# Optimization experiments

Hardware: AMD Instinct MI355X
Metric: run time of the kernel (lower is better)

## Reference

```python
import jax, jax.numpy as jnp
import numpy as np

N_HEADS = 4
D_K = 64
SCALE = D_K ** (-0.5)


def setup_inputs() -> dict:
    key = jax.random.key(0)
    k1, k2, k3, k4, k5 = jax.random.split(key, 5)
    B, C, H, W = 16, 256, 32, 32
    x = jax.random.normal(k1, (B, C, H, W), dtype=jnp.float32)
    # Linear weights stored as (in, out) for x @ W convention
    w_qkv = jax.random.normal(k2, (C, N_HEADS * D_K * 3), dtype=jnp.float32) * (C ** -0.5)
    b_qkv = jax.random.normal(k3, (N_HEADS * D_K * 3,), dtype=jnp.float32) * 0.02
    w_out = jax.random.normal(k4, (N_HEADS * D_K, C), dtype=jnp.float32) * ((N_HEADS * D_K) ** -0.5)
    b_out = jax.random.normal(k5, (C,), dtype=jnp.float32) * 0.02
    return {"x": x, "w_qkv": w_qkv, "b_qkv": b_qkv, "w_out": w_out, "b_out": b_out}


def reference(x, w_qkv, b_qkv, w_out, b_out):
    # NOTE: the original torch module defines GroupNorm but never applies it
    # in forward; we faithfully reproduce the forward as written.
    B, C, H, W = x.shape
    S = H * W
    xs = x.reshape(B, C, S).transpose(0, 2, 1)            # [B, S, C]
    qkv = (xs @ w_qkv + b_qkv).reshape(B, S, N_HEADS, 3 * D_K)
    q, k, v = jnp.split(qkv, 3, axis=-1)                   # each [B, S, H, d_k]
    attn = jnp.einsum('bihd,bjhd->bijh', q, k) * SCALE     # [B, S, S, H]
    attn = jax.nn.softmax(attn, axis=2)                    # softmax over j (keys)
    res = jnp.einsum('bijh,bjhd->bihd', attn, v)           # [B, S, H, d_k]
    res = res.reshape(B, S, N_HEADS * D_K)
    res = res @ w_out + b_out + xs                         # residual add
    return res.transpose(0, 2, 1).reshape(B, C, H, W)
```

## Files before the change

### kernel.cpp

```cpp
#include <hip/hip_runtime.h>
#include <hip/hip_bf16.h>

typedef __attribute__((ext_vector_type(8))) short short8;
typedef __attribute__((ext_vector_type(4))) short short4v;
typedef __attribute__((ext_vector_type(4))) float floatx4;
typedef unsigned short u16;

#define SCL_LOG2E 0.1803368801111204f

__device__ inline u16 f2b(float f) {
  __hip_bfloat16 h = __float2bfloat16(f);
  union { __hip_bfloat16 h; u16 u; } cv; cv.h = h; return cv.u;
}

__global__ __launch_bounds__(256) void qkv_gemm(const float* __restrict__ x,
                                                const float* __restrict__ wq,
                                                const float* __restrict__ bias,
                                                u16* __restrict__ Qo,
                                                u16* __restrict__ Ko,
                                                u16* __restrict__ Vto) {
  __shared__ u16 As[128 * 40];
  __shared__ u16 Bs[128 * 40];
  const int tid = threadIdx.x, wave = tid >> 6, lane = tid & 63;
  const int l15 = lane & 15, quad = lane >> 4;
  const int wm = (wave >> 1) * 64, wn = (wave & 1) * 64;
  const int n0 = blockIdx.x * 128, m0 = blockIdx.y * 128;
  const int bb = m0 >> 10, s0 = m0 & 1023;
  const int c4 = (tid & 7) * 4;
  const int r4 = (tid >> 3) * 4;

  floatx4 acc[4][4] = {};

  for (int kt = 0; kt < 256; kt += 32) {
    const float* xr = x + ((size_t)(bb * 256 + kt + c4)) * 1024 + s0 + r4;
    const float* wr = wq + (size_t)(kt + c4) * 768 + n0 + r4;
    float4 av[4], bv[4];
#pragma unroll
    for (int i = 0; i < 4; i++) {
      av[i] = *(const float4*)&xr[(size_t)i * 1024];
      bv[i] = *(const float4*)&wr[(size_t)i * 768];
    }
#pragma unroll
    for (int j = 0; j < 4; j++) {
      ushort4 pa, pb;
      pa.x = f2b(((const float*)&av[0])[j]);
      pa.y = f2b(((const float*)&av[1])[j]);
      pa.z = f2b(((const float*)&av[2])[j]);
      pa.w = f2b(((const float*)&av[3])[j]);
      pb.x = f2b(((const float*)&bv[0])[j]);
      pb.y = f2b(((const float*)&bv[1])[j]);
      pb.z = f2b(((const float*)&bv[2])[j]);
      pb.w = f2b(((const float*)&bv[3])[j]);
      *(ushort4*)&As[(r4 + j) * 40 + c4] = pa;
      *(ushort4*)&Bs[(r4 + j) * 40 + c4] = pb;
    }
    __syncthreads();
    short8 af[4], bfr[4];
#pragma unroll
    for (int mi = 0; mi < 4; mi++)
      af[mi] = *(short8*)&As[(wm + mi * 16 + l15) * 40 + quad * 8];
#pragma unroll
    for (int ni = 0; ni < 4; ni++)
      bfr[ni] = *(short8*)&Bs[(wn + ni * 16 + l15) * 40 + quad * 8];
#pragma unroll
    for (int mi = 0; mi < 4; mi++)
#pragma unroll
      for (int ni = 0; ni < 4; ni++)
        acc[mi][ni] = __builtin_amdgcn_mfma_f32_16x16x32_bf16(af[mi], bfr[ni],
                                                              acc[mi][ni], 0, 0, 0);
    __syncthreads();
  }

#pragma unroll
  for (int ni = 0; ni < 4; ni++) {
    int n = n0 + wn + ni * 16 + l15;
    float bvv = bias[n];
    int h = n / 192;
    int rem = n - h * 192;
#pragma unroll
    for (int mi = 0; mi < 4; mi++) {
      int gm = m0 + wm + mi * 16 + quad * 4;
      int s = gm & 1023;
      if (rem < 128) {
        u16* dst;
        float scl;
        if (rem < 64) { dst = Qo; scl = SCL_LOG2E; } else { dst = Ko; scl = 1.0f; }
        int d = rem & 63;
#pragma unroll
        for (int r = 0; r < 4; r++)
          dst[((size_t)(bb * 4 + h) * 1024 + s + r) * 64 + d] =
              f2b((acc[mi][ni][r] + bvv) * scl);
      } else {
        int d = rem - 128;
        ushort4 pk;
        pk.x = f2b(acc[mi][ni][0] + bvv);
        pk.y = f2b(acc[mi][ni][1] + bvv);
        pk.z = f2b(acc[mi][ni][2] + bvv);
        pk.w = f2b(acc[mi][ni][3] + bvv);
        *(ushort4*)&Vto[((size_t)(bb * 4 + h) * 64 + d) * 1024 + s] = pk;
      }
    }
  }
}

__global__ __launch_bounds__(256, 2) void attn_kern(const u16* __restrict__ Q,
                                                    const u16* __restrict__ K,
                                                    const u16* __restrict__ Vt,
                                                    u16* __restrict__ O) {
  __shared__ u16 kv[2 * 2 * 64 * 72];
  const int bh = blockIdx.y;
  const u16* Qp = Q + (size_t)bh * 64 * 1024;
  const u16* Kp = K + (size_t)bh * 64 * 1024;
  const u16* Vp = Vt + (size_t)bh * 64 * 1024;
  u16* Op = O + (size_t)bh * 64 * 1024;
  const int q0 = blockIdx.x * 128;
  const int tid = threadIdx.x, wave = tid >> 6, lane = tid & 63;
  const int l15 = lane & 15, quad = lane >> 4;

  short8 qa[2][2];
#pragma unroll
  for (int qi = 0; qi < 2; qi++)
#pragma unroll
    for (int kh = 0; kh < 2; kh++)
      qa[qi][kh] = *(const short8*)&Qp[(size_t)(q0 + wave * 32 + qi * 16 + l15) * 64 +
                                       kh * 32 + quad * 8];

  const int srow = tid >> 2;
  const int sc = (tid & 3) * 16;

  {
    short8 k0 = *(const short8*)&Kp[(size_t)srow * 64 + sc];
    short8 k1 = *(const short8*)&Kp[(size_t)srow * 64 + sc + 8];
    short8 v0 = *(const short8*)&Vp[(size_t)srow * 1024 + sc];
    short8 v1 = *(const short8*)&Vp[(size_t)srow * 1024 + sc + 8];
    *(short8*)&kv[srow * 72 + sc] = k0;
    *(short8*)&kv[srow * 72 + sc + 8] = k1;
    *(short8*)&kv[4608 + srow * 72 + sc] = v0;
    *(short8*)&kv[4608 + srow * 72 + sc + 8] = v1;
  }
  __syncthreads();

  float lsum[2] = {0.f, 0.f};
  floatx4 acc[2][4] = {};

  for (int t = 0; t < 16; t++) {
    const u16* Ksb = kv + (t & 1) * 9216;
    const u16* Vsb = Ksb + 4608;

    short8 nk0, nk1, nv0, nv1;
    if (t < 15) {
      nk0 = *(const short8*)&Kp[(size_t)((t + 1) * 64 + srow) * 64 + sc];
      nk1 = *(const short8*)&Kp[(size_t)((t + 1) * 64 + srow) * 64 + sc + 8];
      nv0 = *(const short8*)&Vp[(size_t)srow * 1024 + (t + 1) * 64 + sc];
      nv1 = *(const short8*)&Vp[(size_t)srow * 1024 + (t + 1) * 64 + sc + 8];
    }

    short8 kb[4][2];
#pragma unroll
    for (int mj = 0; mj < 4; mj++)
#pragma unroll
      for (int kh = 0; kh < 2; kh++)
        kb[mj][kh] = *(const short8*)&Ksb[(mj * 16 + l15) * 72 + kh * 32 + quad * 8];

    floatx4 sf[2][4];
#pragma unroll
    for (int qi = 0; qi < 2; qi++)
#pragma unroll
      for (int mj = 0; mj < 4; mj++) {
        floatx4 z = {};
        z = __builtin_amdgcn_mfma_f32_16x16x32_bf16(kb[mj][0], qa[qi][0], z, 0, 0, 0);
        sf[qi][mj] =
            __builtin_amdgcn_mfma_f32_16x16x32_bf16(kb[mj][1], qa[qi][1], z, 0, 0, 0);
      }

    short4v pb[2][4];
#pragma unroll
    for (int qi = 0; qi < 2; qi++)
#pragma unroll
      for (int mj = 0; mj < 4; mj++) {
        float p0 = exp2f(sf[qi][mj][0]), p1 = exp2f(sf[qi][mj][1]);
        float p2 = exp2f(sf[qi][mj][2]), p3 = exp2f(sf[qi][mj][3]);
        lsum[qi] += (p0 + p1) + (p2 + p3);
        short4v pk;
        pk[0] = (short)f2b(p0); pk[1] = (short)f2b(p1);
        pk[2] = (short)f2b(p2); pk[3] = (short)f2b(p3);
        pb[qi][mj] = pk;
      }

#pragma unroll
    for (int c = 0; c < 4; c++)
#pragma unroll
      for (int md = 0; md < 4; md++) {
        short4v va = *(const short4v*)&Vsb[(md * 16 + l15) * 72 + c * 16 + quad * 4];
#pragma unroll
        for (int qi = 0; qi < 2; qi++)
          acc[qi][md] =
              __builtin_amdgcn_mfma_f32_16x16x16bf16_1k(va, pb[qi][c], acc[qi][md],
                                                        0, 0, 0);
      }

    if (t < 15) {
      u16* dst = kv + ((t + 1) & 1) * 9216;
      *(short8*)&dst[srow * 72 + sc] = nk0;
      *(short8*)&dst[srow * 72 + sc + 8] = nk1;
      *(short8*)&dst[4608 + srow * 72 + sc] = nv0;
      *(short8*)&dst[4608 + srow * 72 + sc + 8] = nv1;
    }
    __syncthreads();
  }

  float inv[2];
#pragma unroll
  for (int qi = 0; qi < 2; qi++) {
    lsum[qi] += __shfl_xor(lsum[qi], 16, 64);
    lsum[qi] += __shfl_xor(lsum[qi], 32, 64);
    inv[qi] = 1.f / lsum[qi];
  }

  __syncthreads();
  u16* Ot = kv;
#pragma unroll
  for (int qi = 0; qi < 2; qi++)
#pragma unroll
    for (int md = 0; md < 4; md++) {
      uint2 pk;
      u16 a0 = f2b(acc[qi][md][0] * inv[qi]), a1 = f2b(acc[qi][md][1] * inv[qi]);
      u16 a2 = f2b(acc[qi][md][2] * inv[qi]), a3 = f2b(acc[qi][md][3] * inv[qi]);
      pk.x = (unsigned)a0 | ((unsigned)a1 << 16);
      pk.y = (unsigned)a2 | ((unsigned)a3 << 16);
      *(uint2*)&Ot[(wave * 32 + qi * 16 + l15) * 72 + md * 16 + quad * 4] = pk;
    }
  __syncthreads();
#pragma unroll
  for (int rr = 0; rr < 4; rr++) {
    int row = wave * 32 + (lane >> 3) + 8 * rr;
    int col = (lane & 7) * 8;
    short8 v = *(const short8*)&Ot[row * 72 + col];
    *(short8*)&Op[(size_t)(q0 + row) * 64 + col] = v;
  }
}

__global__ __launch_bounds__(256) void out_gemm(const u16* __restrict__ Oin,
                                                const float* __restrict__ wo,
                                                const float* __restrict__ bias,
                                                const float* __restrict__ x,
                                                float* __restrict__ out) {
  __shared__ u16 As[64 * 32];
  __shared__ u16 Bs[128 * 40];
  const int tid = threadIdx.x, wave = tid >> 6, lane = tid & 63;
  const int l15 = lane & 15, quad = lane >> 4;
  const int wm = (wave >> 1) * 32, wn = (wave & 1) * 64;
  const int n0 = blockIdx.x * 128, m0 = blockIdx.y * 64;
  const int bb = m0 >> 10, s0 = m0 & 1023;
  const int ar = tid >> 2, ach = (tid & 3) * 8;
  const int c4 = (tid & 7) * 4, r4 = (tid >> 3) * 4;

  floatx4 acc[2][4] = {};

  for (int kt = 0; kt < 256; kt += 32) {
    int h = kt >> 6, d0 = kt & 63;
    *(short8*)&As[ar * 32 + ach] =
        *(const short8*)&Oin[((size_t)(bb * 4 + h) * 1024 + s0 + ar) * 64 + d0 + ach];
    const float* wr = wo + (size_t)(kt + c4) * 256 + n0 + r4;
    float4 bv[4];
#pragma unroll
    for (int i = 0; i < 4; i++) bv[i] = *(const float4*)&wr[(size_t)i * 256];
#pragma unroll
    for (int j = 0; j < 4; j++) {
      ushort4 pb;
      pb.x = f2b(((const float*)&bv[0])[j]);
      pb.y = f2b(((const float*)&bv[1])[j]);
      pb.z = f2b(((const float*)&bv[2])[j]);
      pb.w = f2b(((const float*)&bv[3])[j]);
      *(ushort4*)&Bs[(r4 + j) * 40 + c4] = pb;
    }
    __syncthreads();
    short8 af[2], bfr[4];
#pragma unroll
    for (int mi = 0; mi < 2; mi++)
      af[mi] = *(short8*)&As[(wm + mi * 16 + l15) * 32 + quad * 8];
#pragma unroll
    for (int ni = 0; ni < 4; ni++)
      bfr[ni] = *(short8*)&Bs[(wn + ni * 16 + l15) * 40 + quad * 8];
#pragma unroll
    for (int mi = 0; mi < 2; mi++)
#pragma unroll
      for (int ni = 0; ni < 4; ni++)
        acc[mi][ni] = __builtin_amdgcn_mfma_f32_16x16x32_bf16(af[mi], bfr[ni],
                                                              acc[mi][ni], 0, 0, 0);
    __syncthreads();
  }

#pragma unroll
  for (int ni = 0; ni < 4; ni++) {
    int c = n0 + wn + ni * 16 + l15;
    float bvv = bias[c];
#pragma unroll
    for (int mi = 0; mi < 2; mi++) {
      int gm = m0 + wm + mi * 16 + quad * 4;
      int s = gm & 1023;
      size_t idx = ((size_t)bb * 256 + c) * 1024 + s;
      float4 xr = *(const float4*)&x[idx];
      float4 o;
      o.x = acc[mi][ni][0] + bvv + xr.x;
      o.y = acc[mi][ni][1] + bvv + xr.y;
      o.z = acc[mi][ni][2] + bvv + xr.z;
      o.w = acc[mi][ni][3] + bvv + xr.w;
      *(float4*)&out[idx] = o;
    }
  }
}

extern "C" void kernel_launch(void* const* d_in, const int* in_sizes, int n_in,
                              void* d_out, int out_size, void* d_ws, size_t ws_size,
                              hipStream_t stream) {
  const float* x     = (const float*)d_in[0];
  const float* w_qkv = (const float*)d_in[1];
  const float* b_qkv = (const float*)d_in[2];
  const float* w_out = (const float*)d_in[3];
  const float* b_out = (const float*)d_in[4];
  float* out = (float*)d_out;
  char* ws = (char*)d_ws;

  u16* Qb  = (u16*)(ws);
  u16* Kb  = (u16*)(ws + 8388608);
  u16* Vtb = (u16*)(ws + 16777216);
  u16* Ob  = (u16*)(ws + 25165824);

  qkv_gemm<<<dim3(6, 128), 256, 0, stream>>>(x, w_qkv, b_qkv, Qb, Kb, Vtb);
  attn_kern<<<dim3(8, 64), 256, 0, stream>>>(Qb, Kb, Vtb, Ob);
  out_gemm<<<dim3(2, 256), 256, 0, stream>>>(Ob, w_out, b_out, x, out);
}
```

Baseline: 151.0 us.

## Halve attention query tile per block and swap GEMM grid axes

The attention kernel now processes 64 queries per block (16 per wave) instead of 128, doubling the grid to 1024 blocks and raising the occupancy hint to 4 blocks per CU. This aims to fill more CUs and hide latency, but each K/V tile loaded into shared memory is reused by half as many queries, so K/V traffic roughly doubles. Both GEMMs swap grid axes so consecutive blocks walk along M while sharing the same weight column tile, which should change L2 reuse patterns.

```diff
diff --git a/kernel.cpp b/kernel.cpp
--- a/kernel.cpp
+++ b/kernel.cpp
@@ -24,7 +24,7 @@
   const int tid = threadIdx.x, wave = tid >> 6, lane = tid & 63;
   const int l15 = lane & 15, quad = lane >> 4;
   const int wm = (wave >> 1) * 64, wn = (wave & 1) * 64;
-  const int n0 = blockIdx.x * 128, m0 = blockIdx.y * 128;
+  const int m0 = blockIdx.x * 128, n0 = blockIdx.y * 128;
   const int bb = m0 >> 10, s0 = m0 & 1023;
   const int c4 = (tid & 7) * 4;
   const int r4 = (tid >> 3) * 4;
@@ -103,7 +103,7 @@
   }
 }
 
-__global__ __launch_bounds__(256, 2) void attn_kern(const u16* __restrict__ Q,
+__global__ __launch_bounds__(256, 4) void attn_kern(const u16* __restrict__ Q,
                                                     const u16* __restrict__ K,
                                                     const u16* __restrict__ Vt,
                                                     u16* __restrict__ O) {
@@ -113,17 +113,14 @@
   const u16* Kp = K + (size_t)bh * 64 * 1024;
   const u16* Vp = Vt + (size_t)bh * 64 * 1024;
   u16* Op = O + (size_t)bh * 64 * 1024;
-  const int q0 = blockIdx.x * 128;
+  const int q0 = blockIdx.x * 64;
   const int tid = threadIdx.x, wave = tid >> 6, lane = tid & 63;
   const int l15 = lane & 15, quad = lane >> 4;
 
-  short8 qa[2][2];
-#pragma unroll
-  for (int qi = 0; qi < 2; qi++)
-#pragma unroll
-    for (int kh = 0; kh < 2; kh++)
-      qa[qi][kh] = *(const short8*)&Qp[(size_t)(q0 + wave * 32 + qi * 16 + l15) * 64 +
-                                       kh * 32 + quad * 8];
+  short8 qa[2];
+#pragma unroll
+  for (int kh = 0; kh < 2; kh++)
+    qa[kh] = *(const short8*)&Qp[(size_t)(q0 + wave * 16 + l15) * 64 + kh * 32 + quad * 8];
 
   const int srow = tid >> 2;
   const int sc = (tid & 3) * 16;
@@ -140,8 +137,8 @@
   }
   __syncthreads();
 
-  float lsum[2] = {0.f, 0.f};
-  floatx4 acc[2][4] = {};
+  float lsum = 0.f;
+  floatx4 acc[4] = {};
 
   for (int t = 0; t < 16; t++) {
     const u16* Ksb = kv + (t & 1) * 9216;
@@ -155,48 +152,34 @@
       nv1 = *(const short8*)&Vp[(size_t)srow * 1024 + (t + 1) * 64 + sc + 8];
     }
 
-    short8 kb[4][2];
-#pragma unroll
-    for (int mj = 0; mj < 4; mj++)
-#pragma unroll
-      for (int kh = 0; kh < 2; kh++)
-        kb[mj][kh] = *(const short8*)&Ksb[(mj * 16 + l15) * 72 + kh * 32 + quad * 8];
-
-    floatx4 sf[2][4];
-#pragma unroll
-    for (int qi = 0; qi < 2; qi++)
-#pragma unroll
-      for (int mj = 0; mj < 4; mj++) {
-        floatx4 z = {};
-        z = __builtin_amdgcn_mfma_f32_16x16x32_bf16(kb[mj][0], qa[qi][0], z, 0, 0, 0);
-        sf[qi][mj] =
-            __builtin_amdgcn_mfma_f32_16x16x32_bf16(kb[mj][1], qa[qi][1], z, 0, 0, 0);
-      }
-
-    short4v pb[2][4];
-#pragma unroll
-    for (int qi = 0; qi < 2; qi++)
-#pragma unroll
-      for (int mj = 0; mj < 4; mj++) {
-        float p0 = exp2f(sf[qi][mj][0]), p1 = exp2f(sf[qi][mj][1]);
-        float p2 = exp2f(sf[qi][mj][2]), p3 = exp2f(sf[qi][mj][3]);
-        lsum[qi] += (p0 + p1) + (p2 + p3);
-        short4v pk;
-        pk[0] = (short)f2b(p0); pk[1] = (short)f2b(p1);
-        pk[2] = (short)f2b(p2); pk[3] = (short)f2b(p3);
-        pb[qi][mj] = pk;
-      }
+    floatx4 sf[4];
+#pragma unroll
+    for (int mj = 0; mj < 4; mj++) {
+      short8 kb0 = *(const short8*)&Ksb[(mj * 16 + l15) * 72 + quad * 8];
+      short8 kb1 = *(const short8*)&Ksb[(mj * 16 + l15) * 72 + 32 + quad * 8];
+      floatx4 z = {};
+      z = __builtin_amdgcn_mfma_f32_16x16x32_bf16(kb0, qa[0], z, 0, 0, 0);
+      sf[mj] = __builtin_amdgcn_mfma_f32_16x16x32_bf16(kb1, qa[1], z, 0, 0, 0);
+    }
+
+    short4v pb[4];
+#pragma unroll
+    for (int mj = 0; mj < 4; mj++) {
+      float p0 = exp2f(sf[mj][0]), p1 = exp2f(sf[mj][1]);
+      float p2 = exp2f(sf[mj][2]), p3 = exp2f(sf[mj][3]);
+      lsum += (p0 + p1) + (p2 + p3);
+      short4v pk;
+      pk[0] = (short)f2b(p0); pk[1] = (short)f2b(p1);
+      pk[2] = (short)f2b(p2); pk[3] = (short)f2b(p3);
+      pb[mj] = pk;
+    }
 
 #pragma unroll
     for (int c = 0; c < 4; c++)
 #pragma unroll
       for (int md = 0; md < 4; md++) {
         short4v va = *(const short4v*)&Vsb[(md * 16 + l15) * 72 + c * 16 + quad * 4];
-#pragma unroll
-        for (int qi = 0; qi < 2; qi++)
-          acc[qi][md] =
-              __builtin_amdgcn_mfma_f32_16x16x16bf16_1k(va, pb[qi][c], acc[qi][md],
-                                                        0, 0, 0);
+        acc[md] = __builtin_amdgcn_mfma_f32_16x16x16bf16_1k(va, pb[c], acc[md], 0, 0, 0);
       }
 
     if (t < 15) {
@@ -209,31 +192,25 @@
     __syncthreads();
   }
 
-  float inv[2];
-#pragma unroll
-  for (int qi = 0; qi < 2; qi++) {
-    lsum[qi] += __shfl_xor(lsum[qi], 16, 64);
-    lsum[qi] += __shfl_xor(lsum[qi], 32, 64);
-    inv[qi] = 1.f / lsum[qi];
-  }
+  lsum += __shfl_xor(lsum, 16, 64);
+  lsum += __shfl_xor(lsum, 32, 64);
+  float inv = 1.f / lsum;
 
   __syncthreads();
   u16* Ot = kv;
 #pragma unroll
-  for (int qi = 0; qi < 2; qi++)
-#pragma unroll
-    for (int md = 0; md < 4; md++) {
-      uint2 pk;
-      u16 a0 = f2b(acc[qi][md][0] * inv[qi]), a1 = f2b(acc[qi][md][1] * inv[qi]);
-      u16 a2 = f2b(acc[qi][md][2] * inv[qi]), a3 = f2b(acc[qi][md][3] * inv[qi]);
-      pk.x = (unsigned)a0 | ((unsigned)a1 << 16);
-      pk.y = (unsigned)a2 | ((unsigned)a3 << 16);
-      *(uint2*)&Ot[(wave * 32 + qi * 16 + l15) * 72 + md * 16 + quad * 4] = pk;
-    }
+  for (int md = 0; md < 4; md++) {
+    uint2 pk;
+    u16 a0 = f2b(acc[md][0] * inv), a1 = f2b(acc[md][1] * inv);
+    u16 a2 = f2b(acc[md][2] * inv), a3 = f2b(acc[md][3] * inv);
+    pk.x = (unsigned)a0 | ((unsigned)a1 << 16);
+    pk.y = (unsigned)a2 | ((unsigned)a3 << 16);
+    *(uint2*)&Ot[(wave * 16 + l15) * 72 + md * 16 + quad * 4] = pk;
+  }
   __syncthreads();
 #pragma unroll
-  for (int rr = 0; rr < 4; rr++) {
-    int row = wave * 32 + (lane >> 3) + 8 * rr;
+  for (int h = 0; h < 2; h++) {
+    int row = wave * 16 + h * 8 + (lane >> 3);
     int col = (lane & 7) * 8;
     short8 v = *(const short8*)&Ot[row * 72 + col];
     *(short8*)&Op[(size_t)(q0 + row) * 64 + col] = v;
@@ -250,7 +227,7 @@
   const int tid = threadIdx.x, wave = tid >> 6, lane = tid & 63;
   const int l15 = lane & 15, quad = lane >> 4;
   const int wm = (wave >> 1) * 32, wn = (wave & 1) * 64;
-  const int n0 = blockIdx.x * 128, m0 = blockIdx.y * 64;
+  const int m0 = blockIdx.x * 64, n0 = blockIdx.y * 128;
   const int bb = m0 >> 10, s0 = m0 & 1023;
   const int ar = tid >> 2, ach = (tid & 3) * 8;
   const int c4 = (tid & 7) * 4, r4 = (tid >> 3) * 4;
@@ -327,7 +304,7 @@
   u16* Vtb = (u16*)(ws + 16777216);
   u16* Ob  = (u16*)(ws + 25165824);
 
-  qkv_gemm<<<dim3(6, 128), 256, 0, stream>>>(x, w_qkv, b_qkv, Qb, Kb, Vtb);
-  attn_kern<<<dim3(8, 64), 256, 0, stream>>>(Qb, Kb, Vtb, Ob);
-  out_gemm<<<dim3(2, 256), 256, 0, stream>>>(Ob, w_out, b_out, x, out);
-}
+  qkv_gemm<<<dim3(128, 6), 256, 0, stream>>>(x, w_qkv, b_qkv, Qb, Kb, Vtb);
+  attn_kern<<<dim3(16, 64), 256, 0, stream>>>(Qb, Kb, Vtb, Ob);
+  out_gemm<<<dim3(256, 2), 256, 0, stream>>>(Ob, w_out, b_out, x, out);
+}
```

Measured after the change: 152.7 us. About the same (+1.1%).
